# Performance work log

Hardware: AMD Instinct MI355X
Metric: run time of the kernel (lower is better)

The kernel has to match this reference:

```python
import jax, jax.numpy as jnp
import numpy as np

# Simulates GEMM + intra-node reduce-scatter across `world` ranks on one device.
# Rank r holds A[r]: [M, K_local] and weight[r]: [N, K_local] (K split over ranks).
# Math: reduced = sum_r A[r] @ weight[r]^T  (the all-reduce part),
# then scatter rows: rank r keeps reduced[r*M_per:(r+1)*M_per].

WORLD = 8
M = 8192
N = 2048
K_LOCAL = 256  # K_total = WORLD * K_LOCAL = 2048


def setup_inputs() -> dict:
    key = jax.random.key(0)
    k1, k2 = jax.random.split(key)
    A = jax.random.normal(k1, (WORLD, M, K_LOCAL), dtype=jnp.float32)
    weight = jax.random.normal(k2, (WORLD, N, K_LOCAL), dtype=jnp.float32) * 0.02
    return {"A": A, "weight": weight}


def reference(A, weight):
    world, m, _ = A.shape
    n = weight.shape[1]
    # Fused per-rank GEMM + reduce over ranks: [M, N]
    reduced = jnp.einsum("rmk,rnk->mn", A, weight)
    # Scatter: rank r gets its contiguous M/world row block -> [world, M_per, N]
    m_per = m // world
    return reduced.reshape(world, m_per, n)
```

## Files before the change

kernel.cpp:

```cpp
#include <hip/hip_runtime.h>
#include <hip/hip_bf16.h>

typedef __bf16 bf16x8 __attribute__((ext_vector_type(8)));
typedef __bf16 bf16x4 __attribute__((ext_vector_type(4)));
typedef float f32x4 __attribute__((ext_vector_type(4)));

#define WORLD 8
#define M_DIM 8192
#define N_DIM 2048
#define KL 256
#define K_TOT 2048

#define BM 256
#define BN 256
#define BK 64
#define NT (K_TOT / BK)
#define NITER (NT / 2)

#define AS1 __attribute__((address_space(1)))
#define AS3 __attribute__((address_space(3)))

#define BAR()    __builtin_amdgcn_s_barrier()
#define VMCNT4() asm volatile("s_waitcnt vmcnt(4)" ::: "memory")
#define PRIO1()  __builtin_amdgcn_s_setprio(1)
#define PRIO0()  __builtin_amdgcn_s_setprio(0)

__global__ __launch_bounds__(256) void GemmRS_convert_kernel(
    const float* __restrict__ A,
    const float* __restrict__ W,
    __bf16* __restrict__ Abf,
    __bf16* __restrict__ Wbf)
{
    const long long GA = (long long)WORLD * M_DIM * KL / 4;
    const long long GW = (long long)WORLD * N_DIM * KL / 4;
    const long long stride = (long long)gridDim.x * blockDim.x;
    for (long long g = (long long)blockIdx.x * blockDim.x + threadIdx.x;
         g < GA + GW; g += stride) {
        if (g < GA) {
            const long long e = g * 4;
            const int k = (int)(e & (KL - 1));
            const int m = (int)((e >> 8) & (M_DIM - 1));
            const int r = (int)(e >> 21);
            const float4 v = *reinterpret_cast<const float4*>(A + e);
            bf16x4 o;
            o[0] = (__bf16)v.x; o[1] = (__bf16)v.y;
            o[2] = (__bf16)v.z; o[3] = (__bf16)v.w;
            *reinterpret_cast<bf16x4*>(Abf + (size_t)m * K_TOT + r * KL + k) = o;
        } else {
            const long long e = (g - GA) * 4;
            const int k = (int)(e & (KL - 1));
            const int n = (int)((e >> 8) & (N_DIM - 1));
            const int r = (int)(e >> 19);
            const float4 v = *reinterpret_cast<const float4*>(W + e);
            bf16x4 o;
            o[0] = (__bf16)v.x; o[1] = (__bf16)v.y;
            o[2] = (__bf16)v.z; o[3] = (__bf16)v.w;
            *reinterpret_cast<bf16x4*>(Wbf + (size_t)n * K_TOT + r * KL + k) = o;
        }
    }
}


__device__ __forceinline__ void stage_half(const __bf16* srcbase, __bf16* dstbase,
                                           int lane, int wave) {
    const int rl = lane >> 3;
    const int g  = (lane & 7) ^ rl;
    const __bf16* s = srcbase + (size_t)(wave * 8 + rl) * K_TOT + g * 8;
#pragma unroll
    for (int j = 0; j < 2; ++j) {
        __builtin_amdgcn_global_load_lds(
            (const AS1 void*)(s + (size_t)(j * 64) * K_TOT),
            (AS3 void*)(dstbase + (j * 64 + wave * 8) * BK),
            16, 0, 0);
    }
}

template<int MH>
__device__ __forceinline__ void read_A(bf16x8 (&a)[4][2], const __bf16* Lbase,
                                       int arow, int gk0, int gk1) {
#pragma unroll
    for (int f = 0; f < 4; ++f) {
        const __bf16* rp = Lbase + arow + (MH * 4 + f) * 16 * BK;
        a[f][0] = *reinterpret_cast<const bf16x8*>(rp + gk0);
        a[f][1] = *reinterpret_cast<const bf16x8*>(rp + gk1);
    }
}

template<int F0, int F1>
__device__ __forceinline__ void read_B(bf16x8 (&b)[4][2], const __bf16* Lbase,
                                       int brow, int gk0, int gk1) {
#pragma unroll
    for (int f = F0; f < F1; ++f) {
        const __bf16* rp = Lbase + brow + f * 16 * BK;
        b[f][0] = *reinterpret_cast<const bf16x8*>(rp + gk0);
        b[f][1] = *reinterpret_cast<const bf16x8*>(rp + gk1);
    }
}

template<int MH, int NH>
__device__ __forceinline__ void mma_quad(f32x4 (&acc)[8][4],
                                         bf16x8 (&a)[4][2], bf16x8 (&b)[4][2]) {
#pragma unroll
    for (int ks = 0; ks < 2; ++ks)
#pragma unroll
        for (int f = 0; f < 4; ++f)
#pragma unroll
            for (int j = 0; j < 2; ++j)
                acc[MH * 4 + f][NH * 2 + j] =
                    __builtin_amdgcn_mfma_f32_16x16x32_bf16(
                        a[f][ks], b[NH * 2 + j][ks],
                        acc[MH * 4 + f][NH * 2 + j], 0, 0, 0);
}

__global__ __launch_bounds__(512, 2) void GemmRS_gemm_kernel(
    const __bf16* __restrict__ Abf,
    const __bf16* __restrict__ Wbf,
    float* __restrict__ C)
{
    __shared__ __bf16 lds[2][2][BM * BK];

    const int tid  = threadIdx.x;
    const int lane = tid & 63;
    const int wave = tid >> 6;
    const int wr   = wave >> 2;
    const int wc   = wave & 3;

    const int bid = blockIdx.x;
    const int swz = (bid & 7) * 32 + (bid >> 3);
    const int tm = swz >> 3;
    const int tn = swz & 7;
    const size_t m0 = (size_t)tm * BM;
    const size_t n0 = (size_t)tn * BN;

    const __bf16* aptr = Abf + m0 * K_TOT;
    const __bf16* bptr = Wbf + n0 * K_TOT;

    __bf16* LA0 = &lds[0][0][0];
    __bf16* LB0 = &lds[0][1][0];
    __bf16* LA1 = &lds[1][0][0];
    __bf16* LB1 = &lds[1][1][0];

    auto ST = [&](__bf16* dst, const __bf16* srcp, int h, int t) {
        stage_half(srcp + (size_t)(h * 128) * K_TOT + t * BK,
                   dst + h * 128 * BK, lane, wave);
    };

    const int r15 = lane & 15;
    const int g2  = lane >> 4;
    const int l7  = lane & 7;
    const int gk0 = ((g2)     ^ l7) * 8;
    const int gk1 = ((4 + g2) ^ l7) * 8;
    const int arow = (wr * 128 + r15) * BK;
    const int brow = (wc * 64  + r15) * BK;

    f32x4 acc[8][4];
#pragma unroll
    for (int i = 0; i < 8; ++i)
#pragma unroll
        for (int j = 0; j < 4; ++j)
            acc[i][j] = (f32x4){0.f, 0.f, 0.f, 0.f};

    bf16x8 a[4][2], b[4][2];

    ST(LA0, aptr, 0, 0);
    ST(LA0, aptr, 1, 0);
    ST(LB0, bptr, 0, 0);
    ST(LB0, bptr, 1, 0);
    ST(LB1, bptr, 0, 1);
    ST(LB1, bptr, 1, 1);
    VMCNT4();
    BAR();

    for (int i = 0; i < NITER; ++i) {
        const int t1 = 2 * i + 1;
        const int t2 = (2 * i + 2 < NT) ? 2 * i + 2 : NT - 1;
        const int t3 = (2 * i + 3 < NT) ? 2 * i + 3 : NT - 1;

        read_A<0>(a, LA0, arow, gk0, gk1);
        read_B<0, 2>(b, LB0, brow, gk0, gk1);
        ST(LA1, aptr, 0, t1);
        BAR();
        PRIO1(); mma_quad<0, 0>(acc, a, b); PRIO0();
        read_B<2, 4>(b, LB0, brow, gk0, gk1);
        ST(LA1, aptr, 1, t1);
        BAR();
        PRIO1(); mma_quad<0, 1>(acc, a, b); PRIO0();
        read_A<1>(a, LA0, arow, gk0, gk1);
        ST(LB0, bptr, 0, t2);
        BAR();
        PRIO1(); mma_quad<1, 1>(acc, a, b); PRIO0();
        ST(LB0, bptr, 1, t2);
        BAR();
        PRIO1(); mma_quad<1, 0>(acc, a, b); PRIO0();
        VMCNT4();
        BAR();

        read_A<0>(a, LA1, arow, gk0, gk1);
        read_B<0, 2>(b, LB1, brow, gk0, gk1);
        ST(LA0, aptr, 0, t2);
        BAR();
        PRIO1(); mma_quad<0, 0>(acc, a, b); PRIO0();
        read_B<2, 4>(b, LB1, brow, gk0, gk1);
        ST(LA0, aptr, 1, t2);
        BAR();
        PRIO1(); mma_quad<0, 1>(acc, a, b); PRIO0();
        read_A<1>(a, LA1, arow, gk0, gk1);
        ST(LB1, bptr, 0, t3);
        BAR();
        PRIO1(); mma_quad<1, 1>(acc, a, b); PRIO0();
        ST(LB1, bptr, 1, t3);
        BAR();
        PRIO1(); mma_quad<1, 0>(acc, a, b); PRIO0();
        VMCNT4();
        BAR();
    }

    float* eb = reinterpret_cast<float*>(&lds[0][0][0]) + wave * 1088;
#pragma unroll
    for (int fa = 0; fa < 8; ++fa) {
#pragma unroll
        for (int fb = 0; fb < 4; ++fb)
#pragma unroll
            for (int q = 0; q < 4; ++q)
                eb[(g2 * 4 + q) * 68 + fb * 16 + r15] = acc[fa][fb][q];
#pragma unroll
        for (int j = 0; j < 4; ++j) {
            const int row = j * 4 + g2;
            f32x4 v = *reinterpret_cast<const f32x4*>(eb + row * 68 + r15 * 4);
            *reinterpret_cast<f32x4*>(
                C + (m0 + wr * 128 + fa * 16 + row) * (size_t)N_DIM
                  + n0 + wc * 64 + r15 * 4) = v;
        }
    }
}

extern "C" void kernel_launch(void* const* d_in, const int* in_sizes, int n_in,
                              void* d_out, int out_size, void* d_ws, size_t ws_size,
                              hipStream_t stream) {
    (void)in_sizes; (void)n_in; (void)out_size; (void)ws_size;
    const float* A = (const float*)d_in[0];
    const float* W = (const float*)d_in[1];
    float* C = (float*)d_out;

    __bf16* Abf = (__bf16*)d_ws;
    __bf16* Wbf = (__bf16*)((char*)d_ws + (size_t)M_DIM * K_TOT * 2);

    GemmRS_convert_kernel<<<2048, 256, 0, stream>>>(A, W, Abf, Wbf);
    GemmRS_gemm_kernel<<<(M_DIM / BM) * (N_DIM / BN), 512, 0, stream>>>(Abf, Wbf, C);
}
```

Before: 80.41 us.

## Peel last K iteration and overlap direct output stores with final MFMAs

New measurement: 79.13 us. About the same (-1.6%).

```diff
diff --git a/kernel.cpp b/kernel.cpp
--- a/kernel.cpp
+++ b/kernel.cpp
@@ -22,6 +22,7 @@
 
 #define BAR()    __builtin_amdgcn_s_barrier()
 #define VMCNT4() asm volatile("s_waitcnt vmcnt(4)" ::: "memory")
+#define VMCNT0() asm volatile("s_waitcnt vmcnt(0)" ::: "memory")
 #define PRIO1()  __builtin_amdgcn_s_setprio(1)
 #define PRIO0()  __builtin_amdgcn_s_setprio(0)
 
@@ -112,6 +113,22 @@
                         acc[MH * 4 + f][NH * 2 + j], 0, 0, 0);
 }
 
+template<int FA0, int FB0>
+__device__ __forceinline__ void store_quad(const f32x4 (&acc)[8][4],
+                                           float* __restrict__ C,
+                                           size_t m0, size_t n0,
+                                           int wr, int wc, int g2, int r15) {
+#pragma unroll
+    for (int fa = 0; fa < 4; ++fa)
+#pragma unroll
+        for (int fb = 0; fb < 2; ++fb)
+#pragma unroll
+            for (int q = 0; q < 4; ++q)
+                C[(m0 + wr * 128 + (FA0 + fa) * 16 + g2 * 4 + q) * (size_t)N_DIM
+                  + n0 + wc * 64 + (FB0 + fb) * 16 + r15]
+                    = acc[FA0 + fa][FB0 + fb][q];
+}
+
 __global__ __launch_bounds__(512, 2) void GemmRS_gemm_kernel(
     const __bf16* __restrict__ Abf,
     const __bf16* __restrict__ Wbf,
@@ -171,9 +188,9 @@
     VMCNT4();
     BAR();
 
-    for (int i = 0; i < NITER; ++i) {
+    for (int i = 0; i < NITER - 1; ++i) {
         const int t1 = 2 * i + 1;
-        const int t2 = (2 * i + 2 < NT) ? 2 * i + 2 : NT - 1;
+        const int t2 = 2 * i + 2;
         const int t3 = (2 * i + 3 < NT) ? 2 * i + 3 : NT - 1;
 
         read_A<0>(a, LA0, arow, gk0, gk1);
@@ -215,22 +232,41 @@
         BAR();
     }
 
-    float* eb = reinterpret_cast<float*>(&lds[0][0][0]) + wave * 1088;
-#pragma unroll
-    for (int fa = 0; fa < 8; ++fa) {
-#pragma unroll
-        for (int fb = 0; fb < 4; ++fb)
-#pragma unroll
-            for (int q = 0; q < 4; ++q)
-                eb[(g2 * 4 + q) * 68 + fb * 16 + r15] = acc[fa][fb][q];
-#pragma unroll
-        for (int j = 0; j < 4; ++j) {
-            const int row = j * 4 + g2;
-            f32x4 v = *reinterpret_cast<const f32x4*>(eb + row * 68 + r15 * 4);
-            *reinterpret_cast<f32x4*>(
-                C + (m0 + wr * 128 + fa * 16 + row) * (size_t)N_DIM
-                  + n0 + wc * 64 + r15 * 4) = v;
-        }
+    {
+        const int t1 = NT - 1;
+        read_A<0>(a, LA0, arow, gk0, gk1);
+        read_B<0, 2>(b, LB0, brow, gk0, gk1);
+        ST(LA1, aptr, 0, t1);
+        BAR();
+        PRIO1(); mma_quad<0, 0>(acc, a, b); PRIO0();
+        read_B<2, 4>(b, LB0, brow, gk0, gk1);
+        ST(LA1, aptr, 1, t1);
+        BAR();
+        PRIO1(); mma_quad<0, 1>(acc, a, b); PRIO0();
+        read_A<1>(a, LA0, arow, gk0, gk1);
+        BAR();
+        PRIO1(); mma_quad<1, 1>(acc, a, b); PRIO0();
+        BAR();
+        PRIO1(); mma_quad<1, 0>(acc, a, b); PRIO0();
+        VMCNT0();
+        BAR();
+
+        read_A<0>(a, LA1, arow, gk0, gk1);
+        read_B<0, 2>(b, LB1, brow, gk0, gk1);
+        BAR();
+        PRIO1(); mma_quad<0, 0>(acc, a, b); PRIO0();
+        store_quad<0, 0>(acc, C, m0, n0, wr, wc, g2, r15);
+        read_B<2, 4>(b, LB1, brow, gk0, gk1);
+        BAR();
+        PRIO1(); mma_quad<0, 1>(acc, a, b); PRIO0();
+        store_quad<0, 2>(acc, C, m0, n0, wr, wc, g2, r15);
+        read_A<1>(a, LA1, arow, gk0, gk1);
+        BAR();
+        PRIO1(); mma_quad<1, 1>(acc, a, b); PRIO0();
+        store_quad<4, 2>(acc, C, m0, n0, wr, wc, g2, r15);
+        BAR();
+        PRIO1(); mma_quad<1, 0>(acc, a, b); PRIO0();
+        store_quad<4, 0>(acc, C, m0, n0, wr, wc, g2, r15);
     }
 }
 
```

## Load A fragments directly from global memory and stream epilogue stores

Applied to the files above, without the earlier changes.

After: 185.4 us. 131% more time.

```diff
diff --git a/kernel.cpp b/kernel.cpp
--- a/kernel.cpp
+++ b/kernel.cpp
@@ -15,13 +15,12 @@
 #define BN 256
 #define BK 64
 #define NT (K_TOT / BK)
-#define NITER (NT / 2)
 
 #define AS1 __attribute__((address_space(1)))
 #define AS3 __attribute__((address_space(3)))
 
 #define BAR()    __builtin_amdgcn_s_barrier()
-#define VMCNT4() asm volatile("s_waitcnt vmcnt(4)" ::: "memory")
+#define VMCNT0() asm volatile("s_waitcnt vmcnt(0)" ::: "memory")
 #define PRIO1()  __builtin_amdgcn_s_setprio(1)
 #define PRIO0()  __builtin_amdgcn_s_setprio(0)
 
@@ -76,14 +75,14 @@
 }
 
 template<int MH>
-__device__ __forceinline__ void read_A(bf16x8 (&a)[4][2], const __bf16* Lbase,
-                                       int arow, int gk0, int gk1) {
-#pragma unroll
-    for (int f = 0; f < 4; ++f) {
-        const __bf16* rp = Lbase + arow + (MH * 4 + f) * 16 * BK;
-        a[f][0] = *reinterpret_cast<const bf16x8*>(rp + gk0);
-        a[f][1] = *reinterpret_cast<const bf16x8*>(rp + gk1);
-    }
+__device__ __forceinline__ void read_Ag(bf16x8 (&a)[4][2],
+                                        const __bf16* __restrict__ abase, int t) {
+#pragma unroll
+    for (int f = 0; f < 4; ++f)
+#pragma unroll
+        for (int ks = 0; ks < 2; ++ks)
+            a[f][ks] = *reinterpret_cast<const bf16x8*>(
+                abase + (size_t)((MH * 4 + f) * 16) * K_TOT + t * BK + ks * 32);
 }
 
 template<int F0, int F1>
@@ -112,12 +111,28 @@
                         acc[MH * 4 + f][NH * 2 + j], 0, 0, 0);
 }
 
+template<int FA0, int FB0>
+__device__ __forceinline__ void store_quad(const f32x4 (&acc)[8][4],
+                                           float* __restrict__ C,
+                                           size_t m0, size_t n0,
+                                           int wr, int wc, int g2, int r15) {
+#pragma unroll
+    for (int fa = 0; fa < 4; ++fa)
+#pragma unroll
+        for (int fb = 0; fb < 2; ++fb)
+#pragma unroll
+            for (int q = 0; q < 4; ++q)
+                C[(m0 + wr * 128 + (FA0 + fa) * 16 + g2 * 4 + q) * (size_t)N_DIM
+                  + n0 + wc * 64 + (FB0 + fb) * 16 + r15]
+                    = acc[FA0 + fa][FB0 + fb][q];
+}
+
 __global__ __launch_bounds__(512, 2) void GemmRS_gemm_kernel(
     const __bf16* __restrict__ Abf,
     const __bf16* __restrict__ Wbf,
     float* __restrict__ C)
 {
-    __shared__ __bf16 lds[2][2][BM * BK];
+    __shared__ __bf16 lds[2][BN * BK];
 
     const int tid  = threadIdx.x;
     const int lane = tid & 63;
@@ -132,26 +147,23 @@
     const size_t m0 = (size_t)tm * BM;
     const size_t n0 = (size_t)tn * BN;
 
-    const __bf16* aptr = Abf + m0 * K_TOT;
     const __bf16* bptr = Wbf + n0 * K_TOT;
-
-    __bf16* LA0 = &lds[0][0][0];
-    __bf16* LB0 = &lds[0][1][0];
-    __bf16* LA1 = &lds[1][0][0];
-    __bf16* LB1 = &lds[1][1][0];
-
-    auto ST = [&](__bf16* dst, const __bf16* srcp, int h, int t) {
-        stage_half(srcp + (size_t)(h * 128) * K_TOT + t * BK,
-                   dst + h * 128 * BK, lane, wave);
-    };
 
     const int r15 = lane & 15;
     const int g2  = lane >> 4;
     const int l7  = lane & 7;
     const int gk0 = ((g2)     ^ l7) * 8;
     const int gk1 = ((4 + g2) ^ l7) * 8;
-    const int arow = (wr * 128 + r15) * BK;
-    const int brow = (wc * 64  + r15) * BK;
+    const int brow = (wc * 64 + r15) * BK;
+
+    const __bf16* abase = Abf + (m0 + wr * 128 + r15) * (size_t)K_TOT + g2 * 8;
+
+    auto STB = [&](__bf16* dst, int t) {
+#pragma unroll
+        for (int h = 0; h < 2; ++h)
+            stage_half(bptr + (size_t)(h * 128) * K_TOT + t * BK,
+                       dst + h * 128 * BK, lane, wave);
+    };
 
     f32x4 acc[8][4];
 #pragma unroll
@@ -162,75 +174,47 @@
 
     bf16x8 a[4][2], b[4][2];
 
-    ST(LA0, aptr, 0, 0);
-    ST(LA0, aptr, 1, 0);
-    ST(LB0, bptr, 0, 0);
-    ST(LB0, bptr, 1, 0);
-    ST(LB1, bptr, 0, 1);
-    ST(LB1, bptr, 1, 1);
-    VMCNT4();
+    STB(&lds[0][0], 0);
+    VMCNT0();
     BAR();
 
-    for (int i = 0; i < NITER; ++i) {
-        const int t1 = 2 * i + 1;
-        const int t2 = (2 * i + 2 < NT) ? 2 * i + 2 : NT - 1;
-        const int t3 = (2 * i + 3 < NT) ? 2 * i + 3 : NT - 1;
-
-        read_A<0>(a, LA0, arow, gk0, gk1);
-        read_B<0, 2>(b, LB0, brow, gk0, gk1);
-        ST(LA1, aptr, 0, t1);
+    for (int t = 0; t < NT - 1; ++t) {
+        __bf16* LBc = &lds[t & 1][0];
+        __bf16* LBn = &lds[(t + 1) & 1][0];
+
+        read_Ag<0>(a, abase, t);
+        read_B<0, 2>(b, LBc, brow, gk0, gk1);
         BAR();
         PRIO1(); mma_quad<0, 0>(acc, a, b); PRIO0();
-        read_B<2, 4>(b, LB0, brow, gk0, gk1);
-        ST(LA1, aptr, 1, t1);
+        read_B<2, 4>(b, LBc, brow, gk0, gk1);
         BAR();
         PRIO1(); mma_quad<0, 1>(acc, a, b); PRIO0();
-        read_A<1>(a, LA0, arow, gk0, gk1);
-        ST(LB0, bptr, 0, t2);
+        read_Ag<1>(a, abase, t);
+        STB(LBn, t + 1);
+        BAR();
+        PRIO1(); mma_quad<1, 1>(acc, a, b); mma_quad<1, 0>(acc, a, b); PRIO0();
+        VMCNT0();
+        BAR();
+    }
+
+    {
+        const int t = NT - 1;
+        __bf16* LBc = &lds[t & 1][0];
+        read_Ag<0>(a, abase, t);
+        read_B<0, 2>(b, LBc, brow, gk0, gk1);
+        BAR();
+        PRIO1(); mma_quad<0, 0>(acc, a, b); PRIO0();
+        store_quad<0, 0>(acc, C, m0, n0, wr, wc, g2, r15);
+        read_B<2, 4>(b, LBc, brow, gk0, gk1);
+        BAR();
+        PRIO1(); mma_quad<0, 1>(acc, a, b); PRIO0();
+        store_quad<0, 2>(acc, C, m0, n0, wr, wc, g2, r15);
+        read_Ag<1>(a, abase, t);
         BAR();
         PRIO1(); mma_quad<1, 1>(acc, a, b); PRIO0();
-        ST(LB0, bptr, 1, t2);
-        BAR();
+        store_quad<4, 2>(acc, C, m0, n0, wr, wc, g2, r15);
         PRIO1(); mma_quad<1, 0>(acc, a, b); PRIO0();
-        VMCNT4();
-        BAR();
-
-        read_A<0>(a, LA1, arow, gk0, gk1);
-        read_B<0, 2>(b, LB1, brow, gk0, gk1);
-        ST(LA0, aptr, 0, t2);
-        BAR();
-        PRIO1(); mma_quad<0, 0>(acc, a, b); PRIO0();
-        read_B<2, 4>(b, LB1, brow, gk0, gk1);
-        ST(LA0, aptr, 1, t2);
-        BAR();
-        PRIO1(); mma_quad<0, 1>(acc, a, b); PRIO0();
-        read_A<1>(a, LA1, arow, gk0, gk1);
-        ST(LB1, bptr, 0, t3);
-        BAR();
-        PRIO1(); mma_quad<1, 1>(acc, a, b); PRIO0();
-        ST(LB1, bptr, 1, t3);
-        BAR();
-        PRIO1(); mma_quad<1, 0>(acc, a, b); PRIO0();
-        VMCNT4();
-        BAR();
-    }
-
-    float* eb = reinterpret_cast<float*>(&lds[0][0][0]) + wave * 1088;
-#pragma unroll
-    for (int fa = 0; fa < 8; ++fa) {
-#pragma unroll
-        for (int fb = 0; fb < 4; ++fb)
-#pragma unroll
-            for (int q = 0; q < 4; ++q)
-                eb[(g2 * 4 + q) * 68 + fb * 16 + r15] = acc[fa][fb][q];
-#pragma unroll
-        for (int j = 0; j < 4; ++j) {
-            const int row = j * 4 + g2;
-            f32x4 v = *reinterpret_cast<const f32x4*>(eb + row * 68 + r15 * 4);
-            *reinterpret_cast<f32x4*>(
-                C + (m0 + wr * 128 + fa * 16 + row) * (size_t)N_DIM
-                  + n0 + wc * 64 + r15 * 4) = v;
-        }
+        store_quad<4, 0>(acc, C, m0, n0, wr, wc, g2, r15);
     }
 }
 
```
